# Optimization experiments

Hardware: AMD Instinct MI355X
Metric: run time of the kernel (lower is better)

The kernel has to match this reference:

```python
import jax, jax.numpy as jnp
import numpy as np

N_NODES = 100000
N_EDGES = 1600000
IN_DIM = 512
HEADS = 8
CH = 8
OUT_DIM = 64
NEG_SLOPE = 0.2


def gat_conv(x, src, dst, W, a_src, a_dst, b, n_nodes):
    """PyG-style GATConv (eval mode, add_self_loops handled by caller).
    x: [N, F]; W: [F, H, C]; a_src/a_dst: [H, C]; b: [H*C].
    """
    xh = jnp.einsum('nf,fhc->nhc', x, W)              # [N, H, C]
    al_src = jnp.sum(xh * a_src, axis=-1)              # [N, H]
    al_dst = jnp.sum(xh * a_dst, axis=-1)              # [N, H]
    e = jax.nn.leaky_relu(al_src[src] + al_dst[dst], NEG_SLOPE)  # [E, H]
    # segment softmax over edges grouped by destination node
    emax = jax.ops.segment_max(e, dst, num_segments=n_nodes)     # [N, H]
    ex = jnp.exp(e - emax[dst])
    den = jax.ops.segment_sum(ex, dst, num_segments=n_nodes)     # [N, H]
    alpha = ex / (den[dst] + 1e-16)                    # [E, H]
    msg = xh[src] * alpha[..., None]                   # [E, H, C]
    out = jax.ops.segment_sum(msg, dst, num_segments=n_nodes)    # [N, H, C]
    return out.reshape(n_nodes, -1) + b                # concat heads


def setup_inputs() -> dict:
    key = jax.random.key(0)
    ks = jax.random.split(key, 9)
    x = jax.random.normal(ks[0], (N_NODES, IN_DIM), dtype=jnp.float32)
    edge_index = jax.random.randint(ks[1], (2, N_EDGES), 0, N_NODES, dtype=jnp.int32)
    s1 = 1.0 / np.sqrt(IN_DIM)
    W1 = jax.random.normal(ks[2], (IN_DIM, HEADS, CH), dtype=jnp.float32) * s1
    a1_src = jax.random.normal(ks[3], (HEADS, CH), dtype=jnp.float32) * 0.1
    a1_dst = jax.random.normal(ks[4], (HEADS, CH), dtype=jnp.float32) * 0.1
    b1 = jnp.zeros((HEADS * CH,), dtype=jnp.float32)
    s2 = 1.0 / np.sqrt(HEADS * CH)
    W2 = jax.random.normal(ks[5], (HEADS * CH, 1, OUT_DIM), dtype=jnp.float32) * s2
    a2_src = jax.random.normal(ks[6], (1, OUT_DIM), dtype=jnp.float32) * 0.1
    a2_dst = jax.random.normal(ks[7], (1, OUT_DIM), dtype=jnp.float32) * 0.1
    b2 = jnp.zeros((OUT_DIM,), dtype=jnp.float32)
    return {"x": x, "edge_index": edge_index, "W1": W1, "a1_src": a1_src,
            "a1_dst": a1_dst, "b1": b1, "W2": W2, "a2_src": a2_src,
            "a2_dst": a2_dst, "b2": b2}


def reference(x, edge_index, W1, a1_src, a1_dst, b1, W2, a2_src, a2_dst, b2):
    n = x.shape[0]
    loops = jnp.arange(n, dtype=edge_index.dtype)
    src = jnp.concatenate([edge_index[0], loops])  # add self-loops (PyG default)
    dst = jnp.concatenate([edge_index[1], loops])
    # dropout layers are identity in eval mode
    h = jax.nn.relu(gat_conv(x, src, dst, W1, a1_src, a1_dst, b1, n))
    out = gat_conv(h, src, dst, W2, a2_src, a2_dst, b2, n)
    return jax.nn.log_softmax(out, axis=1)
```

## Files before the change

### kernel.cpp

```cpp
#include <hip/hip_runtime.h>
#include <cstddef>

#define NN 100000
#define NE 1600000
#define IN_DIM 512
#define NEG 0.2f
#define HBLK 521
#define DEGMAX 64

typedef short bf16x8 __attribute__((ext_vector_type(8)));
typedef float f32x4 __attribute__((ext_vector_type(4)));

__device__ __forceinline__ unsigned short f2bf_rne(float f) {
    unsigned u = __builtin_bit_cast(unsigned, f);
    unsigned r = u + 0x7fffu + ((u >> 16) & 1u);
    return (unsigned short)(r >> 16);
}
__device__ __forceinline__ float bf2f(unsigned short h) {
    unsigned u = ((unsigned)h) << 16;
    return __builtin_bit_cast(float, u);
}

__global__ void k_pre(int* __restrict__ cnt,
                      const float* __restrict__ W1, unsigned short* __restrict__ h1,
                      unsigned short* __restrict__ l1) {
    int t = blockIdx.x * blockDim.x + threadIdx.x;
    if (t < NN) cnt[t] = 0;
    if (t < 64 * IN_DIM) {
        int n = t >> 9, k = t & 511;
        float v = W1[k * 64 + n];
        unsigned short h = f2bf_rne(v);
        h1[t] = h;
        l1[t] = f2bf_rne(v - bf2f(h));
    }
}

template <int K, int NH, bool ABF16>
__global__ __launch_bounds__(256, 2) void k_mm_mfma(const void* __restrict__ Ap,
                                                    const unsigned short* __restrict__ Bhi,
                                                    const unsigned short* __restrict__ Blo,
                                                    unsigned short* __restrict__ outbf,
                                                    const float* __restrict__ asv,
                                                    const float* __restrict__ adv,
                                                    float* __restrict__ alsrc,
                                                    float* __restrict__ aldst,
                                                    const int* __restrict__ srcv,
                                                    const int* __restrict__ dstv,
                                                    int* __restrict__ cnt,
                                                    int* __restrict__ csr,
                                                    int fillBlocks) {
    __shared__ __align__(16) unsigned char aRaw[2][64 * 64 * 4];
    __shared__ __align__(16) unsigned short bHi[2][64 * 64];
    __shared__ __align__(16) unsigned short bLo[2][64 * 64];
    int tid = threadIdx.x;
    int mmIdx = blockIdx.x;
    if (fillBlocks > 0) {
        if (((blockIdx.x & 3) == 3) && ((blockIdx.x >> 2) < fillBlocks)) {
            int stride = fillBlocks * 256;
            for (int e = (blockIdx.x >> 2) * 256 + tid; e < NE; e += stride) {
                int d = dstv[e];
                int pos = atomicAdd(&cnt[d], 1);
                if (pos < DEGMAX) csr[(size_t)d * DEGMAX + pos] = srcv[e];
            }
            return;
        }
        int below = (blockIdx.x + 1) >> 2;
        if (below > fillBlocks) below = fillBlocks;
        mmIdx = blockIdx.x - below;
    }
    const int NCH = K / 64;
    int wave = tid >> 6, lane = tid & 63;
    int ln = lane & 15, kg = lane >> 4;
    int brow = mmIdx * 64;
    int r = wave * 16 + ln;
    const float* Af = (const float*)Ap;
    const unsigned short* Ab = (const unsigned short*)Ap;
    f32x4 acc[4] = {};

    auto stage = [&](int c, int buf) {
        if (!ABF16) {
            #pragma unroll
            for (int q = 0; q < 4; ++q) {
                int d = q * 256 + tid;
                int row = d >> 4;
                int s = (d & 15) ^ (row & 15);
                int grow = brow + row;
                if (grow >= NN) grow = NN - 1;
                const float* gp = Af + (size_t)grow * K + c * 64 + s * 4;
                __builtin_amdgcn_global_load_lds(
                    (const __attribute__((address_space(1))) float*)gp,
                    (__attribute__((address_space(3))) float*)((float*)&aRaw[buf][0] + (size_t)d * 4),
                    16, 0, 0);
            }
        } else {
            #pragma unroll
            for (int q = 0; q < 2; ++q) {
                int d = q * 256 + tid;
                int row = d >> 3;
                int s = (d & 7) ^ (row & 7);
                int grow = brow + row;
                if (grow >= NN) grow = NN - 1;
                const unsigned short* gp = Ab + (size_t)grow * K + c * 64 + s * 8;
                __builtin_amdgcn_global_load_lds(
                    (const __attribute__((address_space(1))) unsigned short*)gp,
                    (__attribute__((address_space(3))) unsigned short*)((unsigned short*)&aRaw[buf][0] + (size_t)d * 8),
                    16, 0, 0);
            }
        }
        #pragma unroll
        for (int q = 0; q < 2; ++q) {
            int d = q * 256 + tid;
            int row = d >> 3;
            int s = (d & 7) ^ (row & 7);
            const unsigned short* gh = Bhi + (size_t)row * K + c * 64 + s * 8;
            const unsigned short* gl = Blo + (size_t)row * K + c * 64 + s * 8;
            __builtin_amdgcn_global_load_lds(
                (const __attribute__((address_space(1))) unsigned short*)gh,
                (__attribute__((address_space(3))) unsigned short*)(&bHi[buf][(size_t)d * 8]),
                16, 0, 0);
            __builtin_amdgcn_global_load_lds(
                (const __attribute__((address_space(1))) unsigned short*)gl,
                (__attribute__((address_space(3))) unsigned short*)(&bLo[buf][(size_t)d * 8]),
                16, 0, 0);
        }
    };

    stage(0, 0);
    __syncthreads();
    for (int c = 0; c < NCH; ++c) {
        int buf = c & 1;
        if (c + 1 < NCH) stage(c + 1, buf ^ 1);
        #pragma unroll
        for (int sub = 0; sub < 2; ++sub) {
            int kg8 = sub * 4 + kg;
            bf16x8 ah, al;
            if (!ABF16) {
                int s0 = kg8 * 2;
                const float* base = (const float*)&aRaw[buf][0] + (size_t)r * 64;
                float4 f0 = *reinterpret_cast<const float4*>(base + ((s0) ^ (r & 15)) * 4);
                float4 f1 = *reinterpret_cast<const float4*>(base + ((s0 + 1) ^ (r & 15)) * 4);
                float xs[8] = {f0.x, f0.y, f0.z, f0.w, f1.x, f1.y, f1.z, f1.w};
                #pragma unroll
                for (int j = 0; j < 8; ++j) {
                    unsigned short h = f2bf_rne(xs[j]);
                    ah[j] = (short)h;
                    al[j] = (short)f2bf_rne(xs[j] - bf2f(h));
                }
            } else {
                int slotA = kg8 ^ (r & 7);
                ah = *reinterpret_cast<const bf16x8*>(
                    (const unsigned short*)&aRaw[buf][0] + (size_t)r * 64 + slotA * 8);
            }
            #pragma unroll
            for (int nt = 0; nt < 4; ++nt) {
                int rowB = nt * 16 + ln;
                int slotB = kg8 ^ (rowB & 7);
                bf16x8 bh = *reinterpret_cast<const bf16x8*>(&bHi[buf][rowB * 64 + slotB * 8]);
                bf16x8 bl = *reinterpret_cast<const bf16x8*>(&bLo[buf][rowB * 64 + slotB * 8]);
                acc[nt] = __builtin_amdgcn_mfma_f32_16x16x32_bf16(ah, bh, acc[nt], 0, 0, 0);
                if (!ABF16)
                    acc[nt] = __builtin_amdgcn_mfma_f32_16x16x32_bf16(al, bh, acc[nt], 0, 0, 0);
                acc[nt] = __builtin_amdgcn_mfma_f32_16x16x32_bf16(ah, bl, acc[nt], 0, 0, 0);
            }
        }
        __syncthreads();
    }
    int rbase = brow + wave * 16 + kg * 4;
    #pragma unroll
    for (int nt = 0; nt < 4; ++nt)
        #pragma unroll
        for (int i = 0; i < 4; ++i) {
            int rw = rbase + i;
            if (rw < NN) outbf[(size_t)rw * 64 + nt * 16 + ln] = f2bf_rne(acc[nt][i]);
        }
    if (NH == 8) {
        #pragma unroll
        for (int nt = 0; nt < 4; ++nt) {
            float as = asv[nt * 16 + ln], ad = adv[nt * 16 + ln];
            #pragma unroll
            for (int i = 0; i < 4; ++i) {
                float ps = acc[nt][i] * as;
                float pd = acc[nt][i] * ad;
                ps += __shfl_xor(ps, 1, 64); pd += __shfl_xor(pd, 1, 64);
                ps += __shfl_xor(ps, 2, 64); pd += __shfl_xor(pd, 2, 64);
                ps += __shfl_xor(ps, 4, 64); pd += __shfl_xor(pd, 4, 64);
                if ((lane & 7) == 0) {
                    int row = rbase + i;
                    if (row < NN) {
                        int head = nt * 2 + (ln >> 3);
                        alsrc[row * 8 + head] = ps;
                        aldst[row * 8 + head] = pd;
                    }
                }
            }
        }
    }
}

__global__ void k_agg1(const unsigned short* __restrict__ xh, const float* __restrict__ alsrc,
                       const float* __restrict__ aldst, const int* __restrict__ cnt,
                       const int* __restrict__ csr, const float* __restrict__ b1,
                       const float* __restrict__ W2, const float* __restrict__ a2s,
                       const float* __restrict__ a2d,
                       unsigned short* __restrict__ xh2,
                       float* __restrict__ al2s, float* __restrict__ al2d) {
    __shared__ float w2s[64 * 64];
    __shared__ float hsh[4][64];
    int tid = threadIdx.x;
    #pragma unroll
    for (int q = 0; q < 16; ++q) w2s[q * 256 + tid] = W2[q * 256 + tid];
    int node = blockIdx.x * 4 + (tid >> 6);
    int lane = tid & 63;
    int h = lane >> 3;
    float adst = aldst[node * 8 + h];
    float es = alsrc[node * 8 + h] + adst;
    es = es >= 0.f ? es : NEG * es;
    float mA = es, dA = 1.f, aA = bf2f(xh[(size_t)node * 64 + lane]);
    float mB = -3e38f, dB = 0.f, aB = 0.f;
    int beg = node * DEGMAX;
    int deg = cnt[node];
    if (deg > DEGMAX) deg = DEGMAX;
    int end = beg + deg;
    int j = beg;

    auto upd4 = [&](int s0, int s1, int s2, int s3, float& m, float& d, float& a) {
        float e0 = alsrc[s0 * 8 + h] + adst;
        float e1 = alsrc[s1 * 8 + h] + adst;
        float e2 = alsrc[s2 * 8 + h] + adst;
        float e3 = alsrc[s3 * 8 + h] + adst;
        e0 = e0 >= 0.f ? e0 : NEG * e0;
        e1 = e1 >= 0.f ? e1 : NEG * e1;
        e2 = e2 >= 0.f ? e2 : NEG * e2;
        e3 = e3 >= 0.f ? e3 : NEG * e3;
        float v0 = bf2f(xh[(size_t)s0 * 64 + lane]);
        float v1 = bf2f(xh[(size_t)s1 * 64 + lane]);
        float v2 = bf2f(xh[(size_t)s2 * 64 + lane]);
        float v3 = bf2f(xh[(size_t)s3 * 64 + lane]);
        float nm = fmaxf(fmaxf(fmaxf(e0, e1), fmaxf(e2, e3)), m);
        float sc = __expf(m - nm);
        float w0 = __expf(e0 - nm), w1 = __expf(e1 - nm);
        float w2 = __expf(e2 - nm), w3 = __expf(e3 - nm);
        d = d * sc + (w0 + w1) + (w2 + w3);
        a = a * sc + (w0 * v0 + w1 * v1) + (w2 * v2 + w3 * v3);
        m = nm;
    };

    if (j + 7 < end) {
        int i0 = csr[j], i1 = csr[j + 1], i2 = csr[j + 2], i3 = csr[j + 3];
        int i4 = csr[j + 4], i5 = csr[j + 5], i6 = csr[j + 6], i7 = csr[j + 7];
        j += 8;
        for (; j + 7 < end; j += 8) {
            int n0 = csr[j], n1 = csr[j + 1], n2 = csr[j + 2], n3 = csr[j + 3];
            int n4 = csr[j + 4], n5 = csr[j + 5], n6 = csr[j + 6], n7 = csr[j + 7];
            upd4(i0, i1, i2, i3, mA, dA, aA);
            upd4(i4, i5, i6, i7, mB, dB, aB);
            i0 = n0; i1 = n1; i2 = n2; i3 = n3;
            i4 = n4; i5 = n5; i6 = n6; i7 = n7;
        }
        upd4(i0, i1, i2, i3, mA, dA, aA);
        upd4(i4, i5, i6, i7, mB, dB, aB);
    }
    for (; j + 3 < end; j += 4)
        upd4(csr[j], csr[j + 1], csr[j + 2], csr[j + 3], mA, dA, aA);
    for (; j < end; ++j) {
        int s = csr[j];
        float e = alsrc[s * 8 + h] + adst;
        e = e >= 0.f ? e : NEG * e;
        float xv = bf2f(xh[(size_t)s * 64 + lane]);
        float nm = fmaxf(mA, e);
        float sc = __expf(mA - nm);
        float w = __expf(e - nm);
        dA = dA * sc + w;
        aA = aA * sc + w * xv;
        mA = nm;
    }
    {
        float nm = fmaxf(mA, mB);
        float sA = __expf(mA - nm), sB = __expf(mB - nm);
        dA = dA * sA + dB * sB;
        aA = aA * sA + aB * sB;
    }
    float r = aA / (dA + 1e-16f) + b1[lane];
    r = fmaxf(r, 0.f);
    hsh[tid >> 6][lane] = bf2f(f2bf_rne(r));
    __syncthreads();
    float o = 0.f;
    const float* hr = hsh[tid >> 6];
    #pragma unroll 8
    for (int k = 0; k < 64; ++k) o += hr[k] * w2s[k * 64 + lane];
    xh2[(size_t)node * 64 + lane] = f2bf_rne(o);
    float ps = o * a2s[lane], pd = o * a2d[lane];
    #pragma unroll
    for (int off = 1; off < 64; off <<= 1) {
        ps += __shfl_xor(ps, off, 64);
        pd += __shfl_xor(pd, off, 64);
    }
    if (lane == 0) { al2s[node] = ps; al2d[node] = pd; }
}

__global__ void k_agg2(const unsigned short* __restrict__ xh, const float* __restrict__ alsrc,
                       const float* __restrict__ aldst, const int* __restrict__ cnt,
                       const int* __restrict__ csr, const float* __restrict__ b2,
                       float* __restrict__ out) {
    int node = blockIdx.x * 4 + (threadIdx.x >> 6);
    int lane = threadIdx.x & 63;
    if (node >= NN) return;
    float adst = aldst[node];
    float es = alsrc[node] + adst;
    es = es >= 0.f ? es : NEG * es;
    float mA = es, dA = 1.f, aA = bf2f(xh[(size_t)node * 64 + lane]);
    float mB = -3e38f, dB = 0.f, aB = 0.f;
    int beg = node * DEGMAX;
    int deg = cnt[node];
    if (deg > DEGMAX) deg = DEGMAX;
    int end = beg + deg;
    int j = beg;

    auto upd4 = [&](int s0, int s1, int s2, int s3, float& m, float& d, float& a) {
        float e0 = alsrc[s0] + adst;
        float e1 = alsrc[s1] + adst;
        float e2 = alsrc[s2] + adst;
        float e3 = alsrc[s3] + adst;
        e0 = e0 >= 0.f ? e0 : NEG * e0;
        e1 = e1 >= 0.f ? e1 : NEG * e1;
        e2 = e2 >= 0.f ? e2 : NEG * e2;
        e3 = e3 >= 0.f ? e3 : NEG * e3;
        float v0 = bf2f(xh[(size_t)s0 * 64 + lane]);
        float v1 = bf2f(xh[(size_t)s1 * 64 + lane]);
        float v2 = bf2f(xh[(size_t)s2 * 64 + lane]);
        float v3 = bf2f(xh[(size_t)s3 * 64 + lane]);
        float nm = fmaxf(fmaxf(fmaxf(e0, e1), fmaxf(e2, e3)), m);
        float sc = __expf(m - nm);
        float w0 = __expf(e0 - nm), w1 = __expf(e1 - nm);
        float w2 = __expf(e2 - nm), w3 = __expf(e3 - nm);
        d = d * sc + (w0 + w1) + (w2 + w3);
        a = a * sc + (w0 * v0 + w1 * v1) + (w2 * v2 + w3 * v3);
        m = nm;
    };

    if (j + 7 < end) {
        int i0 = csr[j], i1 = csr[j + 1], i2 = csr[j + 2], i3 = csr[j + 3];
        int i4 = csr[j + 4], i5 = csr[j + 5], i6 = csr[j + 6], i7 = csr[j + 7];
        j += 8;
        for (; j + 7 < end; j += 8) {
            int n0 = csr[j], n1 = csr[j + 1], n2 = csr[j + 2], n3 = csr[j + 3];
            int n4 = csr[j + 4], n5 = csr[j + 5], n6 = csr[j + 6], n7 = csr[j + 7];
            upd4(i0, i1, i2, i3, mA, dA, aA);
            upd4(i4, i5, i6, i7, mB, dB, aB);
            i0 = n0; i1 = n1; i2 = n2; i3 = n3;
            i4 = n4; i5 = n5; i6 = n6; i7 = n7;
        }
        upd4(i0, i1, i2, i3, mA, dA, aA);
        upd4(i4, i5, i6, i7, mB, dB, aB);
    }
    for (; j + 3 < end; j += 4)
        upd4(csr[j], csr[j + 1], csr[j + 2], csr[j + 3], mA, dA, aA);
    for (; j < end; ++j) {
        int s = csr[j];
        float e = alsrc[s] + adst;
        e = e >= 0.f ? e : NEG * e;
        float xv = bf2f(xh[(size_t)s * 64 + lane]);
        float nm = fmaxf(mA, e);
        float sc = __expf(mA - nm);
        float w = __expf(e - nm);
        dA = dA * sc + w;
        aA = aA * sc + w * xv;
        mA = nm;
    }
    {
        float nm = fmaxf(mA, mB);
        float sA = __expf(mA - nm), sB = __expf(mB - nm);
        dA = dA * sA + dB * sB;
        aA = aA * sA + aB * sB;
    }
    float v = aA / (dA + 1e-16f) + b2[lane];
    float mx = v;
    #pragma unroll
    for (int off = 1; off < 64; off <<= 1) mx = fmaxf(mx, __shfl_xor(mx, off, 64));
    float ex = __expf(v - mx);
    float s = ex;
    #pragma unroll
    for (int off = 1; off < 64; off <<= 1) s += __shfl_xor(s, off, 64);
    out[(size_t)node * 64 + lane] = v - mx - __logf(s);
}

extern "C" void kernel_launch(void* const* d_in, const int* in_sizes, int n_in,
                              void* d_out, int out_size, void* d_ws, size_t ws_size,
                              hipStream_t stream) {
    const float* x   = (const float*)d_in[0];
    const int*   ei  = (const int*)d_in[1];
    const float* W1  = (const float*)d_in[2];
    const float* a1s = (const float*)d_in[3];
    const float* a1d = (const float*)d_in[4];
    const float* b1  = (const float*)d_in[5];
    const float* W2  = (const float*)d_in[6];
    const float* a2s = (const float*)d_in[7];
    const float* a2d = (const float*)d_in[8];
    const float* b2  = (const float*)d_in[9];
    float* out = (float*)d_out;
    const int* srcv = ei;
    const int* dstv = ei + NE;

    char* w = (char*)d_ws;
    auto alloc = [&](size_t bytes) {
        void* p = (void*)w;
        w += (bytes + 255) & ~(size_t)255;
        return p;
    };
    unsigned short* xh1 = (unsigned short*)alloc((size_t)NN * 64 * 2);
    unsigned short* xh2 = (unsigned short*)alloc((size_t)NN * 64 * 2);
    float* al1s  = (float*)alloc((size_t)NN * 8 * 4);
    float* al1d  = (float*)alloc((size_t)NN * 8 * 4);
    float* al2s  = (float*)alloc((size_t)NN * 4);
    float* al2d  = (float*)alloc((size_t)NN * 4);
    int* cnt     = (int*)alloc((size_t)NN * 4);
    int* csr     = (int*)alloc((size_t)NN * DEGMAX * 4);
    unsigned short* Wb1h = (unsigned short*)alloc((size_t)64 * IN_DIM * 2);
    unsigned short* Wb1l = (unsigned short*)alloc((size_t)64 * IN_DIM * 2);

    const int MMB = (NN + 63) / 64;

    k_pre<<<(NN + 255) / 256, 256, 0, stream>>>(cnt, W1, Wb1h, Wb1l);

    k_mm_mfma<IN_DIM, 8, false><<<MMB + HBLK, 256, 0, stream>>>(x, Wb1h, Wb1l, xh1,
                                                                a1s, a1d, al1s, al1d,
                                                                srcv, dstv, cnt, csr, HBLK);

    k_agg1<<<NN / 4, 256, 0, stream>>>(xh1, al1s, al1d, cnt, csr, b1,
                                       W2, a2s, a2d, xh2, al2s, al2d);

    k_agg2<<<NN / 4, 256, 0, stream>>>(xh2, al2s, al2d, cnt, csr, b2, out);
}
```

Measured before the change: 340.4 us.

## Drop double buffering in first GEMM to halve LDS and raise occupancy

Replaces the templated double-buffered MFMA GEMM with a specialised single-buffer kernel for the fp32-input layer. LDS per block falls from about 64KB to 32KB and launch bounds go from 2 to 4 blocks per CU, so more waves can hide memory latency. The cost is that prefetch of the next K chunk no longer overlaps the compute on the current chunk, and the loop now waits at a barrier after each load. The template branches are also removed.

```diff
diff --git a/kernel.cpp b/kernel.cpp
--- a/kernel.cpp
+++ b/kernel.cpp
@@ -35,77 +35,55 @@
     }
 }
 
-template <int K, int NH, bool ABF16>
-__global__ __launch_bounds__(256, 2) void k_mm_mfma(const void* __restrict__ Ap,
-                                                    const unsigned short* __restrict__ Bhi,
-                                                    const unsigned short* __restrict__ Blo,
-                                                    unsigned short* __restrict__ outbf,
-                                                    const float* __restrict__ asv,
-                                                    const float* __restrict__ adv,
-                                                    float* __restrict__ alsrc,
-                                                    float* __restrict__ aldst,
-                                                    const int* __restrict__ srcv,
-                                                    const int* __restrict__ dstv,
-                                                    int* __restrict__ cnt,
-                                                    int* __restrict__ csr,
-                                                    int fillBlocks) {
-    __shared__ __align__(16) unsigned char aRaw[2][64 * 64 * 4];
-    __shared__ __align__(16) unsigned short bHi[2][64 * 64];
-    __shared__ __align__(16) unsigned short bLo[2][64 * 64];
+__global__ __launch_bounds__(256, 4) void k_mm1(const float* __restrict__ A,
+                                                const unsigned short* __restrict__ Bhi,
+                                                const unsigned short* __restrict__ Blo,
+                                                unsigned short* __restrict__ outbf,
+                                                const float* __restrict__ asv,
+                                                const float* __restrict__ adv,
+                                                float* __restrict__ alsrc,
+                                                float* __restrict__ aldst,
+                                                const int* __restrict__ srcv,
+                                                const int* __restrict__ dstv,
+                                                int* __restrict__ cnt,
+                                                int* __restrict__ csr) {
+    __shared__ __align__(16) float aLds[64 * 64];
+    __shared__ __align__(16) unsigned short bHi[64 * 64];
+    __shared__ __align__(16) unsigned short bLo[64 * 64];
+    const int K = IN_DIM;
     int tid = threadIdx.x;
-    int mmIdx = blockIdx.x;
-    if (fillBlocks > 0) {
-        if (((blockIdx.x & 3) == 3) && ((blockIdx.x >> 2) < fillBlocks)) {
-            int stride = fillBlocks * 256;
-            for (int e = (blockIdx.x >> 2) * 256 + tid; e < NE; e += stride) {
-                int d = dstv[e];
-                int pos = atomicAdd(&cnt[d], 1);
-                if (pos < DEGMAX) csr[(size_t)d * DEGMAX + pos] = srcv[e];
-            }
-            return;
-        }
-        int below = (blockIdx.x + 1) >> 2;
-        if (below > fillBlocks) below = fillBlocks;
-        mmIdx = blockIdx.x - below;
-    }
-    const int NCH = K / 64;
+    if (((blockIdx.x & 3) == 3) && ((blockIdx.x >> 2) < HBLK)) {
+        int stride = HBLK * 256;
+        for (int e = (blockIdx.x >> 2) * 256 + tid; e < NE; e += stride) {
+            int d = dstv[e];
+            int pos = atomicAdd(&cnt[d], 1);
+            if (pos < DEGMAX) csr[(size_t)d * DEGMAX + pos] = srcv[e];
+        }
+        return;
+    }
+    int below = (blockIdx.x + 1) >> 2;
+    if (below > HBLK) below = HBLK;
+    int mmIdx = blockIdx.x - below;
+
     int wave = tid >> 6, lane = tid & 63;
     int ln = lane & 15, kg = lane >> 4;
     int brow = mmIdx * 64;
     int r = wave * 16 + ln;
-    const float* Af = (const float*)Ap;
-    const unsigned short* Ab = (const unsigned short*)Ap;
     f32x4 acc[4] = {};
 
-    auto stage = [&](int c, int buf) {
-        if (!ABF16) {
-            #pragma unroll
-            for (int q = 0; q < 4; ++q) {
-                int d = q * 256 + tid;
-                int row = d >> 4;
-                int s = (d & 15) ^ (row & 15);
-                int grow = brow + row;
-                if (grow >= NN) grow = NN - 1;
-                const float* gp = Af + (size_t)grow * K + c * 64 + s * 4;
-                __builtin_amdgcn_global_load_lds(
-                    (const __attribute__((address_space(1))) float*)gp,
-                    (__attribute__((address_space(3))) float*)((float*)&aRaw[buf][0] + (size_t)d * 4),
-                    16, 0, 0);
-            }
-        } else {
-            #pragma unroll
-            for (int q = 0; q < 2; ++q) {
-                int d = q * 256 + tid;
-                int row = d >> 3;
-                int s = (d & 7) ^ (row & 7);
-                int grow = brow + row;
-                if (grow >= NN) grow = NN - 1;
-                const unsigned short* gp = Ab + (size_t)grow * K + c * 64 + s * 8;
-                __builtin_amdgcn_global_load_lds(
-                    (const __attribute__((address_space(1))) unsigned short*)gp,
-                    (__attribute__((address_space(3))) unsigned short*)((unsigned short*)&aRaw[buf][0] + (size_t)d * 8),
-                    16, 0, 0);
-            }
+    for (int c = 0; c < K / 64; ++c) {
+        #pragma unroll
+        for (int q = 0; q < 4; ++q) {
+            int d = q * 256 + tid;
+            int row = d >> 4;
+            int s = (d & 15) ^ (row & 15);
+            int grow = brow + row;
+            if (grow >= NN) grow = NN - 1;
+            const float* gp = A + (size_t)grow * K + c * 64 + s * 4;
+            __builtin_amdgcn_global_load_lds(
+                (const __attribute__((address_space(1))) float*)gp,
+                (__attribute__((address_space(3))) float*)(aLds + (size_t)d * 4),
+                16, 0, 0);
         }
         #pragma unroll
         for (int q = 0; q < 2; ++q) {
@@ -116,50 +94,37 @@
             const unsigned short* gl = Blo + (size_t)row * K + c * 64 + s * 8;
             __builtin_amdgcn_global_load_lds(
                 (const __attribute__((address_space(1))) unsigned short*)gh,
-                (__attribute__((address_space(3))) unsigned short*)(&bHi[buf][(size_t)d * 8]),
+                (__attribute__((address_space(3))) unsigned short*)(bHi + (size_t)d * 8),
                 16, 0, 0);
             __builtin_amdgcn_global_load_lds(
                 (const __attribute__((address_space(1))) unsigned short*)gl,
-                (__attribute__((address_space(3))) unsigned short*)(&bLo[buf][(size_t)d * 8]),
+                (__attribute__((address_space(3))) unsigned short*)(bLo + (size_t)d * 8),
                 16, 0, 0);
         }
-    };
-
-    stage(0, 0);
-    __syncthreads();
-    for (int c = 0; c < NCH; ++c) {
-        int buf = c & 1;
-        if (c + 1 < NCH) stage(c + 1, buf ^ 1);
+        __syncthreads();
         #pragma unroll
         for (int sub = 0; sub < 2; ++sub) {
             int kg8 = sub * 4 + kg;
+            int s0 = kg8 * 2;
+            const float* base = aLds + (size_t)r * 64;
+            float4 f0 = *reinterpret_cast<const float4*>(base + ((s0) ^ (r & 15)) * 4);
+            float4 f1 = *reinterpret_cast<const float4*>(base + ((s0 + 1) ^ (r & 15)) * 4);
+            float xs[8] = {f0.x, f0.y, f0.z, f0.w, f1.x, f1.y, f1.z, f1.w};
             bf16x8 ah, al;
-            if (!ABF16) {
-                int s0 = kg8 * 2;
-                const float* base = (const float*)&aRaw[buf][0] + (size_t)r * 64;
-                float4 f0 = *reinterpret_cast<const float4*>(base + ((s0) ^ (r & 15)) * 4);
-                float4 f1 = *reinterpret_cast<const float4*>(base + ((s0 + 1) ^ (r & 15)) * 4);
-                float xs[8] = {f0.x, f0.y, f0.z, f0.w, f1.x, f1.y, f1.z, f1.w};
-                #pragma unroll
-                for (int j = 0; j < 8; ++j) {
-                    unsigned short h = f2bf_rne(xs[j]);
-                    ah[j] = (short)h;
-                    al[j] = (short)f2bf_rne(xs[j] - bf2f(h));
-                }
-            } else {
-                int slotA = kg8 ^ (r & 7);
-                ah = *reinterpret_cast<const bf16x8*>(
-                    (const unsigned short*)&aRaw[buf][0] + (size_t)r * 64 + slotA * 8);
+            #pragma unroll
+            for (int j = 0; j < 8; ++j) {
+                unsigned short h = f2bf_rne(xs[j]);
+                ah[j] = (short)h;
+                al[j] = (short)f2bf_rne(xs[j] - bf2f(h));
             }
             #pragma unroll
             for (int nt = 0; nt < 4; ++nt) {
                 int rowB = nt * 16 + ln;
                 int slotB = kg8 ^ (rowB & 7);
-                bf16x8 bh = *reinterpret_cast<const bf16x8*>(&bHi[buf][rowB * 64 + slotB * 8]);
-                bf16x8 bl = *reinterpret_cast<const bf16x8*>(&bLo[buf][rowB * 64 + slotB * 8]);
+                bf16x8 bh = *reinterpret_cast<const bf16x8*>(bHi + rowB * 64 + slotB * 8);
+                bf16x8 bl = *reinterpret_cast<const bf16x8*>(bLo + rowB * 64 + slotB * 8);
                 acc[nt] = __builtin_amdgcn_mfma_f32_16x16x32_bf16(ah, bh, acc[nt], 0, 0, 0);
-                if (!ABF16)
-                    acc[nt] = __builtin_amdgcn_mfma_f32_16x16x32_bf16(al, bh, acc[nt], 0, 0, 0);
+                acc[nt] = __builtin_amdgcn_mfma_f32_16x16x32_bf16(al, bh, acc[nt], 0, 0, 0);
                 acc[nt] = __builtin_amdgcn_mfma_f32_16x16x32_bf16(ah, bl, acc[nt], 0, 0, 0);
             }
         }
@@ -173,24 +138,22 @@
             int rw = rbase + i;
             if (rw < NN) outbf[(size_t)rw * 64 + nt * 16 + ln] = f2bf_rne(acc[nt][i]);
         }
-    if (NH == 8) {
-        #pragma unroll
-        for (int nt = 0; nt < 4; ++nt) {
-            float as = asv[nt * 16 + ln], ad = adv[nt * 16 + ln];
-            #pragma unroll
-            for (int i = 0; i < 4; ++i) {
-                float ps = acc[nt][i] * as;
-                float pd = acc[nt][i] * ad;
-                ps += __shfl_xor(ps, 1, 64); pd += __shfl_xor(pd, 1, 64);
-                ps += __shfl_xor(ps, 2, 64); pd += __shfl_xor(pd, 2, 64);
-                ps += __shfl_xor(ps, 4, 64); pd += __shfl_xor(pd, 4, 64);
-                if ((lane & 7) == 0) {
-                    int row = rbase + i;
-                    if (row < NN) {
-                        int head = nt * 2 + (ln >> 3);
-                        alsrc[row * 8 + head] = ps;
-                        aldst[row * 8 + head] = pd;
-                    }
+    #pragma unroll
+    for (int nt = 0; nt < 4; ++nt) {
+        float as = asv[nt * 16 + ln], ad = adv[nt * 16 + ln];
+        #pragma unroll
+        for (int i = 0; i < 4; ++i) {
+            float ps = acc[nt][i] * as;
+            float pd = acc[nt][i] * ad;
+            ps += __shfl_xor(ps, 1, 64); pd += __shfl_xor(pd, 1, 64);
+            ps += __shfl_xor(ps, 2, 64); pd += __shfl_xor(pd, 2, 64);
+            ps += __shfl_xor(ps, 4, 64); pd += __shfl_xor(pd, 4, 64);
+            if ((lane & 7) == 0) {
+                int row = rbase + i;
+                if (row < NN) {
+                    int head = nt * 2 + (ln >> 3);
+                    alsrc[row * 8 + head] = ps;
+                    aldst[row * 8 + head] = pd;
                 }
             }
         }
@@ -422,9 +385,8 @@
 
     k_pre<<<(NN + 255) / 256, 256, 0, stream>>>(cnt, W1, Wb1h, Wb1l);
 
-    k_mm_mfma<IN_DIM, 8, false><<<MMB + HBLK, 256, 0, stream>>>(x, Wb1h, Wb1l, xh1,
-                                                                a1s, a1d, al1s, al1d,
-                                                                srcv, dstv, cnt, csr, HBLK);
+    k_mm1<<<MMB + HBLK, 256, 0, stream>>>(x, Wb1h, Wb1l, xh1, a1s, a1d, al1s, al1d,
+                                          srcv, dstv, cnt, csr);
 
     k_agg1<<<NN / 4, 256, 0, stream>>>(xh1, al1s, al1d, cnt, csr, b1,
                                        W2, a2s, a2d, xh2, al2s, al2d);
```

Result: faster. 326.6 us (-4.1%).
